# Kernel optimization log

Hardware: AMD Instinct MI355X
Metric: run time of the kernel (lower is better)

Reference implementation:

```python
import jax, jax.numpy as jnp
import numpy as np

D = 128          # cfg_node_encoding_dim
N_NODES = 300000
EPS = 1e-9


def setup_inputs() -> dict:
    key = jax.random.key(0)
    ks = jax.random.split(key, 10)
    inp = {
        "occ_ngram3": jax.random.normal(ks[0], (250000, 3, D), dtype=jnp.float32),
        "idx_ngram3": jax.random.randint(ks[1], (250000, 3), 0, N_NODES, dtype=jnp.int64),
        "occ_ngram5": jax.random.normal(ks[2], (200000, 5, D), dtype=jnp.float32),
        "idx_ngram5": jax.random.randint(ks[3], (200000, 5), 0, N_NODES, dtype=jnp.int64),
        "previous_cfg_nodes_encodings": jax.random.normal(ks[4], (N_NODES, D), dtype=jnp.float32),
        # learned params: attention key projection + GRU-like gate
        "attn_W": jax.random.normal(ks[5], (D, D), dtype=jnp.float32) / np.sqrt(D),
        "attn_b": jnp.zeros((D,), dtype=jnp.float32),
        "gate_W": jax.random.normal(ks[6], (2 * D, D), dtype=jnp.float32) / np.sqrt(2 * D),
        "gate_b": jnp.zeros((D,), dtype=jnp.float32),
        "nr_cfg_nodes": N_NODES,
    }
    return inp


def _scatter_attn_gate(occ3, occ5, prev, attn_W, attn_b, gate_W, gate_b, idx3, idx5, n_nodes):
    # flatten(0,1) + cat over sorted ngram lengths -> [E, D] values, [E] indices
    vals = jnp.concatenate([occ3.reshape(-1, D), occ5.reshape(-1, D)], axis=0)
    idx = jnp.concatenate([idx3.reshape(-1), idx5.reshape(-1)], axis=0)

    # scatter-attention keyed on previous node encodings
    keys = prev @ attn_W + attn_b                        # [N, D]
    scores = jnp.einsum('ed,ed->e', vals, keys[idx]) / jnp.sqrt(jnp.asarray(D, vals.dtype))
    seg_max = jax.ops.segment_max(scores, idx, num_segments=n_nodes)   # -inf for empty segs
    ex = jnp.exp(scores - seg_max[idx])
    denom = jax.ops.segment_sum(ex, idx, num_segments=n_nodes)
    probs = ex / (denom[idx] + EPS)                      # segment softmax [E]
    agg = jax.ops.segment_sum(probs[:, None] * vals, idx, num_segments=n_nodes)  # [N, D]

    # GRU-like gate: z = sigmoid(W [prev; update]); new = z*update + (1-z)*prev
    z = jax.nn.sigmoid(jnp.concatenate([prev, agg], axis=-1) @ gate_W + gate_b)
    return z * agg + (1.0 - z) * prev


def reference(occ_ngram3, idx_ngram3, occ_ngram5, idx_ngram5,
              previous_cfg_nodes_encodings, attn_W, attn_b, gate_W, gate_b,
              nr_cfg_nodes):
    return _scatter_attn_gate(occ_ngram3, occ_ngram5, previous_cfg_nodes_encodings,
                              attn_W, attn_b, gate_W, gate_b,
                              idx_ngram3, idx_ngram5, nr_cfg_nodes)
```

## Files before the change

### kernel.cpp

```cpp
#include <hip/hip_runtime.h>
#include <math.h>

#define D 128
#define EPSF 1e-9f

typedef __bf16 bf16x8 __attribute__((ext_vector_type(8)));
typedef float  f32x4  __attribute__((ext_vector_type(4)));
typedef float  f32x2  __attribute__((ext_vector_type(2)));

static __device__ __forceinline__ float bf2f(unsigned short h) {
    union { unsigned int u; float f; } c; c.u = ((unsigned int)h) << 16;
    return c.f;
}
static __device__ __forceinline__ unsigned short f2bf(float f) {
    union { float f; unsigned int u; } c; c.f = f;
    unsigned int u = c.u + 0x7fffu + ((c.u >> 16) & 1u);
    return (unsigned short)(u >> 16);
}

__global__ __launch_bounds__(256) void transpose_w_kernel(
    const float* __restrict__ attn_W, const float* __restrict__ gate_W,
    __bf16* __restrict__ wta, __bf16* __restrict__ wtg)
{
    int i = blockIdx.x * 256 + threadIdx.x;
    if (i < 128 * 128) {
        int k = i >> 7, n = i & 127;
        wta[n * 128 + k] = (__bf16)attn_W[i];
    }
    if (i < 256 * 128) {
        int k = i >> 7, n = i & 127;
        wtg[n * 256 + k] = (__bf16)gate_W[i];
    }
}

__global__ __launch_bounds__(256) void keys_mfma_kernel(
    const float* __restrict__ prev, const __bf16* __restrict__ wta,
    const float* __restrict__ attn_b, unsigned short* __restrict__ keysb, int N)
{
    const int lane = threadIdx.x & 63;
    const int wid  = threadIdx.x >> 6;
    const int m0 = (blockIdx.x * 4 + wid) * 16;
    if (m0 >= N) return;
    const int lm = lane & 15;
    const int lg = lane >> 4;

    int arow = m0 + lm; if (arow >= N) arow = m0;
    const float* ap = prev + (size_t)arow * D + lg * 8;

    f32x4 acc[8] = {};
    #pragma unroll
    for (int kk = 0; kk < 4; ++kk) {
        float4 a0 = *(const float4*)(ap + kk * 32);
        float4 a1 = *(const float4*)(ap + kk * 32 + 4);
        bf16x8 af;
        af[0] = (__bf16)a0.x; af[1] = (__bf16)a0.y; af[2] = (__bf16)a0.z; af[3] = (__bf16)a0.w;
        af[4] = (__bf16)a1.x; af[5] = (__bf16)a1.y; af[6] = (__bf16)a1.z; af[7] = (__bf16)a1.w;
        const int k0 = kk * 32;
        #pragma unroll
        for (int t = 0; t < 8; ++t) {
            bf16x8 bf_ = *(const bf16x8*)(wta + (size_t)(t * 16 + lm) * 128 + k0 + lg * 8);
            acc[t] = __builtin_amdgcn_mfma_f32_16x16x32_bf16(af, bf_, acc[t], 0, 0, 0);
        }
    }
    __bf16* kb = (__bf16*)keysb;
    #pragma unroll
    for (int t = 0; t < 8; ++t) {
        float bcol = attn_b[t * 16 + lm];
        #pragma unroll
        for (int r = 0; r < 4; ++r) {
            int row = m0 + lg * 4 + r;
            if (row < N)
                kb[(size_t)row * D + t * 16 + lm] = (__bf16)(acc[t][r] + bcol);
        }
    }
}

__global__ __launch_bounds__(256) void hist_kernel(
    const int* __restrict__ idx3, const int* __restrict__ idx5,
    int* __restrict__ cnt, int E3, int E)
{
    int e = blockIdx.x * 256 + threadIdx.x;
    if (e >= E) return;
    int n = (e < E3) ? idx3[e] : idx5[e - E3];
    atomicAdd(&cnt[n], 1);
}

__global__ __launch_bounds__(256) void scan1_kernel(
    const int* __restrict__ cnt, int* __restrict__ row_start,
    int* __restrict__ bsum, int N)
{
    __shared__ int tsum[256];
    const int t = threadIdx.x;
    const int base = blockIdx.x * 1024;
    const int i0 = base + t * 4;
    int v0 = 0, v1 = 0, v2 = 0, v3 = 0;
    if (i0 + 0 < N) v0 = cnt[i0 + 0];
    if (i0 + 1 < N) v1 = cnt[i0 + 1];
    if (i0 + 2 < N) v2 = cnt[i0 + 2];
    if (i0 + 3 < N) v3 = cnt[i0 + 3];
    int s = v0 + v1 + v2 + v3;
    tsum[t] = s;
    __syncthreads();
    int val = s;
    for (int off = 1; off < 256; off <<= 1) {
        int tmp = (t >= off) ? tsum[t - off] : 0;
        __syncthreads();
        val += tmp; tsum[t] = val;
        __syncthreads();
    }
    int excl = val - s;
    if (i0 + 0 < N) row_start[i0 + 0] = excl;            excl += v0;
    if (i0 + 1 < N) row_start[i0 + 1] = excl;            excl += v1;
    if (i0 + 2 < N) row_start[i0 + 2] = excl;            excl += v2;
    if (i0 + 3 < N) row_start[i0 + 3] = excl;
    if (t == 255) bsum[blockIdx.x] = val;
}

__global__ __launch_bounds__(1024) void scan2_kernel(int* __restrict__ bsum, int nb)
{
    __shared__ int sh[1024];
    const int t = threadIdx.x;
    int v = (t < nb) ? bsum[t] : 0;
    sh[t] = v;
    __syncthreads();
    int val = v;
    for (int off = 1; off < 1024; off <<= 1) {
        int tmp = (t >= off) ? sh[t - off] : 0;
        __syncthreads();
        val += tmp; sh[t] = val;
        __syncthreads();
    }
    if (t < nb) bsum[t] = val - v;
}

__global__ __launch_bounds__(256) void scan3_kernel(
    int* __restrict__ row_start, const int* __restrict__ bsum, int N, int E)
{
    int i = blockIdx.x * 256 + threadIdx.x;
    if (i < N)       row_start[i] += bsum[i >> 10];
    else if (i == N) row_start[N] = E;
}

__global__ __launch_bounds__(256) void scatter_kernel(
    const int* __restrict__ idx3, const int* __restrict__ idx5,
    const int* __restrict__ row_start, int* __restrict__ cursor,
    int* __restrict__ edge_ids, int E3, int E)
{
    int e = blockIdx.x * 256 + threadIdx.x;
    if (e >= E) return;
    int n = (e < E3) ? idx3[e] : idx5[e - E3];
    int p = row_start[n] + atomicAdd(&cursor[n], 1);
    edge_ids[p] = e;
}

__global__ __launch_bounds__(256) void agg_kernel(
    const float* __restrict__ occ3, const float* __restrict__ occ5,
    const unsigned short* __restrict__ keysb,
    const int* __restrict__ row_start, const int* __restrict__ edge_ids,
    unsigned int* __restrict__ aggb, int E3, int N)
{
    const int lane = threadIdx.x & 63;
    const int wid  = threadIdx.x >> 6;
    const int n = blockIdx.x * 4 + wid;
    if (n >= N) return;

    unsigned int kp = ((const unsigned int*)keysb)[(size_t)n * (D / 2) + lane];
    float kx = bf2f((unsigned short)(kp & 0xffffu));
    float ky = bf2f((unsigned short)(kp >> 16));

    const int rs = row_start[n];
    const int re = row_start[n + 1];
    const float scale = 0.0883883476483184f;

    float ax = 0.f, ay = 0.f, den = 0.f;

    for (int base = rs; base < re; base += 64) {
        const int nid = re - base;
        const int cnt = nid < 64 ? nid : 64;
        int myid = (lane < cnt) ? edge_ids[base + lane] : 0;

        for (int j0 = 0; j0 < cnt; j0 += 8) {
            f32x2 v[8];
            #pragma unroll
            for (int j = 0; j < 8; ++j) {
                int e = __shfl(myid, j0 + j);
                const f32x2* vp = (e < E3)
                    ? (const f32x2*)(occ3 + (size_t)e * D)
                    : (const f32x2*)(occ5 + (size_t)(e - E3) * D);
                v[j] = __builtin_nontemporal_load(&vp[lane]);
            }
            float s[8];
            #pragma unroll
            for (int j = 0; j < 8; ++j)
                s[j] = v[j][0] * kx + v[j][1] * ky;
            #pragma unroll
            for (int sh = 32; sh >= 1; sh >>= 1) {
                #pragma unroll
                for (int j = 0; j < 8; ++j)
                    s[j] += __shfl_xor(s[j], sh);
            }
            #pragma unroll
            for (int j = 0; j < 8; ++j) {
                float ex = (j0 + j < cnt) ? __expf(s[j] * scale) : 0.f;
                den += ex;
                ax = fmaf(ex, v[j][0], ax);
                ay = fmaf(ex, v[j][1], ay);
            }
        }
    }

    float inv = 1.0f / (den + EPSF);
    unsigned int pack = (unsigned int)f2bf(ax * inv)
                      | ((unsigned int)f2bf(ay * inv) << 16);
    aggb[(size_t)n * (D / 2) + lane] = pack;
}

__global__ __launch_bounds__(256) void gate_mfma_kernel(
    const float* __restrict__ prev, const __bf16* __restrict__ aggb,
    const __bf16* __restrict__ wtg, const float* __restrict__ gate_b,
    float* __restrict__ out, int N)
{
    const int lane = threadIdx.x & 63;
    const int wid  = threadIdx.x >> 6;
    const int m0 = (blockIdx.x * 4 + wid) * 16;
    if (m0 >= N) return;
    const int lm = lane & 15;
    const int lg = lane >> 4;

    int arow = m0 + lm; if (arow >= N) arow = m0;
    const float*  aprev = prev + (size_t)arow * D + lg * 8;
    const __bf16* aagg  = aggb + (size_t)arow * D + lg * 8;

    f32x4 acc[8] = {};
    #pragma unroll
    for (int kk = 0; kk < 4; ++kk) {
        float4 a0 = *(const float4*)(aprev + kk * 32);
        float4 a1 = *(const float4*)(aprev + kk * 32 + 4);
        bf16x8 af;
        af[0] = (__bf16)a0.x; af[1] = (__bf16)a0.y; af[2] = (__bf16)a0.z; af[3] = (__bf16)a0.w;
        af[4] = (__bf16)a1.x; af[5] = (__bf16)a1.y; af[6] = (__bf16)a1.z; af[7] = (__bf16)a1.w;
        const int k0 = kk * 32;
        #pragma unroll
        for (int t = 0; t < 8; ++t) {
            bf16x8 bf_ = *(const bf16x8*)(wtg + (size_t)(t * 16 + lm) * 256 + k0 + lg * 8);
            acc[t] = __builtin_amdgcn_mfma_f32_16x16x32_bf16(af, bf_, acc[t], 0, 0, 0);
        }
    }
    #pragma unroll
    for (int kk = 0; kk < 4; ++kk) {
        bf16x8 af = *(const bf16x8*)(aagg + kk * 32);
        const int k0 = 128 + kk * 32;
        #pragma unroll
        for (int t = 0; t < 8; ++t) {
            bf16x8 bf_ = *(const bf16x8*)(wtg + (size_t)(t * 16 + lm) * 256 + k0 + lg * 8);
            acc[t] = __builtin_amdgcn_mfma_f32_16x16x32_bf16(af, bf_, acc[t], 0, 0, 0);
        }
    }

    const unsigned short* aggu = (const unsigned short*)aggb;
    #pragma unroll
    for (int t = 0; t < 8; ++t) {
        float bcol = gate_b[t * 16 + lm];
        #pragma unroll
        for (int r = 0; r < 4; ++r) {
            int row = m0 + lg * 4 + r;
            if (row < N) {
                size_t off = (size_t)row * D + t * 16 + lm;
                float c = acc[t][r] + bcol;
                float z = 1.0f / (1.0f + __expf(-c));
                float a = bf2f(aggu[off]);
                float p = prev[off];
                out[off] = fmaf(z, a - p, p);
            }
        }
    }
}

extern "C" void kernel_launch(void* const* d_in, const int* in_sizes, int n_in,
                              void* d_out, int out_size, void* d_ws, size_t ws_size,
                              hipStream_t stream)
{
    const float* occ3   = (const float*)d_in[0];
    const int*   idx3   = (const int*)d_in[1];
    const float* occ5   = (const float*)d_in[2];
    const int*   idx5   = (const int*)d_in[3];
    const float* prev   = (const float*)d_in[4];
    const float* attn_W = (const float*)d_in[5];
    const float* attn_b = (const float*)d_in[6];
    const float* gate_W = (const float*)d_in[7];
    const float* gate_b = (const float*)d_in[8];

    const int N  = in_sizes[4] / D;
    const int E3 = in_sizes[1];
    const int E5 = in_sizes[3];
    const int E  = E3 + E5;

    unsigned short* keysb = (unsigned short*)d_ws;
    unsigned int*   aggb  = (unsigned int*)(keysb + (size_t)N * D);
    int* row_start = (int*)((unsigned short*)aggb + (size_t)N * D);
    int* cnt       = row_start + (N + 1);
    int* cursor    = cnt + N;
    int* bsum      = cursor + N;
    int* edge_ids  = bsum + 1025;
    __bf16* wta    = (__bf16*)(edge_ids + E);
    __bf16* wtg    = wta + 128 * 128;

    float* out = (float*)d_out;

    (void)hipMemsetAsync(cnt, 0, (size_t)2 * N * sizeof(int), stream);

    transpose_w_kernel<<<128, 256, 0, stream>>>(attn_W, gate_W, wta, wtg);

    const int nb = (N + 1023) / 1024;
    hist_kernel   <<<(E + 255) / 256, 256, 0, stream>>>(idx3, idx5, cnt, E3, E);
    scan1_kernel  <<<nb, 256, 0, stream>>>(cnt, row_start, bsum, N);
    scan2_kernel  <<<1, 1024, 0, stream>>>(bsum, nb);
    scan3_kernel  <<<(N + 256) / 256, 256, 0, stream>>>(row_start, bsum, N, E);
    scatter_kernel<<<(E + 255) / 256, 256, 0, stream>>>(idx3, idx5, row_start, cursor, edge_ids, E3, E);

    keys_mfma_kernel<<<(N + 63) / 64, 256, 0, stream>>>(prev, wta, attn_b, keysb, N);

    agg_kernel<<<(N + 3) / 4, 256, 0, stream>>>(occ3, occ5, keysb, row_start, edge_ids, aggb, E3, N);

    gate_mfma_kernel<<<(N + 63) / 64, 256, 0, stream>>>(prev, (const __bf16*)aggb, wtg, gate_b, out, N);
}
```

Baseline: 792.1 us.

## Fuse key projection, segment aggregation and gate into one per-tile kernel

Replaces the separate keys, aggregation and gate kernels with one fused kernel. Each wavefront owns 16 consecutive nodes: it computes their keys with MFMA into LDS, walks the CSR edges of all 16 nodes together, accumulates softmax-weighted values with LDS atomics, normalizes, and then runs the gate MFMA reading aggregates from LDS. This removes the global round trips for the bf16 keys and aggregates plus two launches. In exchange it adds LDS atomics, a binary search per edge chunk, and fewer wavefronts for the memory-bound edge gather (one wave per 16 nodes instead of one per node), which may reduce latency hiding.

```diff
diff --git a/kernel.cpp b/kernel.cpp
--- a/kernel.cpp
+++ b/kernel.cpp
@@ -3,6 +3,7 @@
 
 #define D 128
 #define EPSF 1e-9f
+#define KST 136
 
 typedef __bf16 bf16x8 __attribute__((ext_vector_type(8)));
 typedef float  f32x4  __attribute__((ext_vector_type(4)));
@@ -30,48 +31,6 @@
     if (i < 256 * 128) {
         int k = i >> 7, n = i & 127;
         wtg[n * 256 + k] = (__bf16)gate_W[i];
-    }
-}
-
-__global__ __launch_bounds__(256) void keys_mfma_kernel(
-    const float* __restrict__ prev, const __bf16* __restrict__ wta,
-    const float* __restrict__ attn_b, unsigned short* __restrict__ keysb, int N)
-{
-    const int lane = threadIdx.x & 63;
-    const int wid  = threadIdx.x >> 6;
-    const int m0 = (blockIdx.x * 4 + wid) * 16;
-    if (m0 >= N) return;
-    const int lm = lane & 15;
-    const int lg = lane >> 4;
-
-    int arow = m0 + lm; if (arow >= N) arow = m0;
-    const float* ap = prev + (size_t)arow * D + lg * 8;
-
-    f32x4 acc[8] = {};
-    #pragma unroll
-    for (int kk = 0; kk < 4; ++kk) {
-        float4 a0 = *(const float4*)(ap + kk * 32);
-        float4 a1 = *(const float4*)(ap + kk * 32 + 4);
-        bf16x8 af;
-        af[0] = (__bf16)a0.x; af[1] = (__bf16)a0.y; af[2] = (__bf16)a0.z; af[3] = (__bf16)a0.w;
-        af[4] = (__bf16)a1.x; af[5] = (__bf16)a1.y; af[6] = (__bf16)a1.z; af[7] = (__bf16)a1.w;
-        const int k0 = kk * 32;
-        #pragma unroll
-        for (int t = 0; t < 8; ++t) {
-            bf16x8 bf_ = *(const bf16x8*)(wta + (size_t)(t * 16 + lm) * 128 + k0 + lg * 8);
-            acc[t] = __builtin_amdgcn_mfma_f32_16x16x32_bf16(af, bf_, acc[t], 0, 0, 0);
-        }
-    }
-    __bf16* kb = (__bf16*)keysb;
-    #pragma unroll
-    for (int t = 0; t < 8; ++t) {
-        float bcol = attn_b[t * 16 + lm];
-        #pragma unroll
-        for (int r = 0; r < 4; ++r) {
-            int row = m0 + lg * 4 + r;
-            if (row < N)
-                kb[(size_t)row * D + t * 16 + lm] = (__bf16)(acc[t][r] + bcol);
-        }
     }
 }
 
@@ -153,73 +112,18 @@
     edge_ids[p] = e;
 }
 
-__global__ __launch_bounds__(256) void agg_kernel(
+__global__ __launch_bounds__(256) void fused_kernel(
+    const float* __restrict__ prev,
     const float* __restrict__ occ3, const float* __restrict__ occ5,
-    const unsigned short* __restrict__ keysb,
+    const __bf16* __restrict__ wta, const __bf16* __restrict__ wtg,
+    const float* __restrict__ attn_b, const float* __restrict__ gate_b,
     const int* __restrict__ row_start, const int* __restrict__ edge_ids,
-    unsigned int* __restrict__ aggb, int E3, int N)
-{
-    const int lane = threadIdx.x & 63;
-    const int wid  = threadIdx.x >> 6;
-    const int n = blockIdx.x * 4 + wid;
-    if (n >= N) return;
-
-    unsigned int kp = ((const unsigned int*)keysb)[(size_t)n * (D / 2) + lane];
-    float kx = bf2f((unsigned short)(kp & 0xffffu));
-    float ky = bf2f((unsigned short)(kp >> 16));
-
-    const int rs = row_start[n];
-    const int re = row_start[n + 1];
-    const float scale = 0.0883883476483184f;
-
-    float ax = 0.f, ay = 0.f, den = 0.f;
-
-    for (int base = rs; base < re; base += 64) {
-        const int nid = re - base;
-        const int cnt = nid < 64 ? nid : 64;
-        int myid = (lane < cnt) ? edge_ids[base + lane] : 0;
-
-        for (int j0 = 0; j0 < cnt; j0 += 8) {
-            f32x2 v[8];
-            #pragma unroll
-            for (int j = 0; j < 8; ++j) {
-                int e = __shfl(myid, j0 + j);
-                const f32x2* vp = (e < E3)
-                    ? (const f32x2*)(occ3 + (size_t)e * D)
-                    : (const f32x2*)(occ5 + (size_t)(e - E3) * D);
-                v[j] = __builtin_nontemporal_load(&vp[lane]);
-            }
-            float s[8];
-            #pragma unroll
-            for (int j = 0; j < 8; ++j)
-                s[j] = v[j][0] * kx + v[j][1] * ky;
-            #pragma unroll
-            for (int sh = 32; sh >= 1; sh >>= 1) {
-                #pragma unroll
-                for (int j = 0; j < 8; ++j)
-                    s[j] += __shfl_xor(s[j], sh);
-            }
-            #pragma unroll
-            for (int j = 0; j < 8; ++j) {
-                float ex = (j0 + j < cnt) ? __expf(s[j] * scale) : 0.f;
-                den += ex;
-                ax = fmaf(ex, v[j][0], ax);
-                ay = fmaf(ex, v[j][1], ay);
-            }
-        }
-    }
-
-    float inv = 1.0f / (den + EPSF);
-    unsigned int pack = (unsigned int)f2bf(ax * inv)
-                      | ((unsigned int)f2bf(ay * inv) << 16);
-    aggb[(size_t)n * (D / 2) + lane] = pack;
-}
-
-__global__ __launch_bounds__(256) void gate_mfma_kernel(
-    const float* __restrict__ prev, const __bf16* __restrict__ aggb,
-    const __bf16* __restrict__ wtg, const float* __restrict__ gate_b,
-    float* __restrict__ out, int N)
-{
+    float* __restrict__ out, int E3, int N)
+{
+    __shared__ __bf16 kag[4][16 * KST];
+    __shared__ float  agf[4][16 * D];
+    __shared__ float  dnf[4][16];
+
     const int lane = threadIdx.x & 63;
     const int wid  = threadIdx.x >> 6;
     const int m0 = (blockIdx.x * 4 + wid) * 16;
@@ -227,50 +131,140 @@
     const int lm = lane & 15;
     const int lg = lane >> 4;
 
+    __bf16* kl = kag[wid];
+    float*  af = agf[wid];
+    float*  dn = dnf[wid];
+
+    for (int i = lane; i < 16 * D; i += 64) af[i] = 0.f;
+    if (lane < 16) dn[lane] = 0.f;
+
     int arow = m0 + lm; if (arow >= N) arow = m0;
-    const float*  aprev = prev + (size_t)arow * D + lg * 8;
-    const __bf16* aagg  = aggb + (size_t)arow * D + lg * 8;
-
-    f32x4 acc[8] = {};
+    const float* ap = prev + (size_t)arow * D + lg * 8;
+    {
+        f32x4 acc[8] = {};
+        #pragma unroll
+        for (int kk = 0; kk < 4; ++kk) {
+            float4 a0 = *(const float4*)(ap + kk * 32);
+            float4 a1 = *(const float4*)(ap + kk * 32 + 4);
+            bf16x8 afr;
+            afr[0] = (__bf16)a0.x; afr[1] = (__bf16)a0.y; afr[2] = (__bf16)a0.z; afr[3] = (__bf16)a0.w;
+            afr[4] = (__bf16)a1.x; afr[5] = (__bf16)a1.y; afr[6] = (__bf16)a1.z; afr[7] = (__bf16)a1.w;
+            const int k0 = kk * 32;
+            #pragma unroll
+            for (int t = 0; t < 8; ++t) {
+                bf16x8 bfr = *(const bf16x8*)(wta + (size_t)(t * 16 + lm) * 128 + k0 + lg * 8);
+                acc[t] = __builtin_amdgcn_mfma_f32_16x16x32_bf16(afr, bfr, acc[t], 0, 0, 0);
+            }
+        }
+        #pragma unroll
+        for (int t = 0; t < 8; ++t) {
+            float b = attn_b[t * 16 + lm];
+            #pragma unroll
+            for (int r = 0; r < 4; ++r)
+                kl[(lg * 4 + r) * KST + t * 16 + lm] = (__bf16)(acc[t][r] + b);
+        }
+    }
+
+    const int rs0 = row_start[m0];
+    int hi = m0 + 16; if (hi > N) hi = N;
+    const int re0 = row_start[hi];
+    int bidx = m0 + (lane < 16 ? lane : 16); if (bidx > N) bidx = N;
+    const int rsv = row_start[bidx];
+    const float scale = 0.0883883476483184f;
+
+    for (int base = rs0; base < re0; base += 64) {
+        int cnt = re0 - base; if (cnt > 64) cnt = 64;
+        int p = base + lane;
+        int myid = (lane < cnt) ? edge_ids[p] : 0;
+        int lo = 0;
+        #pragma unroll
+        for (int st = 8; st >= 1; st >>= 1) {
+            int v = __shfl(rsv, lo + st);
+            if (v <= p) lo += st;
+        }
+
+        for (int q0 = 0; q0 < cnt; q0 += 8) {
+            f32x2 v[8]; int nl[8]; float s[8];
+            #pragma unroll
+            for (int j = 0; j < 8; ++j) {
+                int e = __shfl(myid, q0 + j);
+                nl[j] = __shfl(lo, q0 + j);
+                const f32x2* vp = (e < E3)
+                    ? (const f32x2*)(occ3 + (size_t)e * D)
+                    : (const f32x2*)(occ5 + (size_t)(e - E3) * D);
+                v[j] = __builtin_nontemporal_load(&vp[lane]);
+            }
+            #pragma unroll
+            for (int j = 0; j < 8; ++j) {
+                unsigned int kp = *(const unsigned int*)(kl + nl[j] * KST + 2 * lane);
+                s[j] = v[j][0] * bf2f((unsigned short)(kp & 0xffffu))
+                     + v[j][1] * bf2f((unsigned short)(kp >> 16));
+            }
+            #pragma unroll
+            for (int sh = 32; sh >= 1; sh >>= 1) {
+                #pragma unroll
+                for (int j = 0; j < 8; ++j)
+                    s[j] += __shfl_xor(s[j], sh);
+            }
+            #pragma unroll
+            for (int j = 0; j < 8; ++j) {
+                float ex = (q0 + j < cnt) ? __expf(s[j] * scale) : 0.f;
+                atomicAdd(&af[nl[j] * D + 2 * lane],     ex * v[j][0]);
+                atomicAdd(&af[nl[j] * D + 2 * lane + 1], ex * v[j][1]);
+                if (lane == 0) atomicAdd(&dn[nl[j]], ex);
+            }
+        }
+    }
+    __threadfence_block();
+
+    #pragma unroll
+    for (int i = 0; i < 16; ++i) {
+        float inv = 1.0f / (dn[i] + EPSF);
+        float x = af[i * D + 2 * lane] * inv;
+        float y = af[i * D + 2 * lane + 1] * inv;
+        unsigned int pk = (unsigned int)f2bf(x) | ((unsigned int)f2bf(y) << 16);
+        *(unsigned int*)(kl + i * KST + 2 * lane) = pk;
+    }
+
+    f32x4 gacc[8] = {};
     #pragma unroll
     for (int kk = 0; kk < 4; ++kk) {
-        float4 a0 = *(const float4*)(aprev + kk * 32);
-        float4 a1 = *(const float4*)(aprev + kk * 32 + 4);
-        bf16x8 af;
-        af[0] = (__bf16)a0.x; af[1] = (__bf16)a0.y; af[2] = (__bf16)a0.z; af[3] = (__bf16)a0.w;
-        af[4] = (__bf16)a1.x; af[5] = (__bf16)a1.y; af[6] = (__bf16)a1.z; af[7] = (__bf16)a1.w;
+        float4 a0 = *(const float4*)(ap + kk * 32);
+        float4 a1 = *(const float4*)(ap + kk * 32 + 4);
+        bf16x8 afr;
+        afr[0] = (__bf16)a0.x; afr[1] = (__bf16)a0.y; afr[2] = (__bf16)a0.z; afr[3] = (__bf16)a0.w;
+        afr[4] = (__bf16)a1.x; afr[5] = (__bf16)a1.y; afr[6] = (__bf16)a1.z; afr[7] = (__bf16)a1.w;
         const int k0 = kk * 32;
         #pragma unroll
         for (int t = 0; t < 8; ++t) {
-            bf16x8 bf_ = *(const bf16x8*)(wtg + (size_t)(t * 16 + lm) * 256 + k0 + lg * 8);
-            acc[t] = __builtin_amdgcn_mfma_f32_16x16x32_bf16(af, bf_, acc[t], 0, 0, 0);
+            bf16x8 bfr = *(const bf16x8*)(wtg + (size_t)(t * 16 + lm) * 256 + k0 + lg * 8);
+            gacc[t] = __builtin_amdgcn_mfma_f32_16x16x32_bf16(afr, bfr, gacc[t], 0, 0, 0);
         }
     }
     #pragma unroll
     for (int kk = 0; kk < 4; ++kk) {
-        bf16x8 af = *(const bf16x8*)(aagg + kk * 32);
+        bf16x8 afr = *(const bf16x8*)(kl + lm * KST + kk * 32 + lg * 8);
         const int k0 = 128 + kk * 32;
         #pragma unroll
         for (int t = 0; t < 8; ++t) {
-            bf16x8 bf_ = *(const bf16x8*)(wtg + (size_t)(t * 16 + lm) * 256 + k0 + lg * 8);
-            acc[t] = __builtin_amdgcn_mfma_f32_16x16x32_bf16(af, bf_, acc[t], 0, 0, 0);
-        }
-    }
-
-    const unsigned short* aggu = (const unsigned short*)aggb;
+            bf16x8 bfr = *(const bf16x8*)(wtg + (size_t)(t * 16 + lm) * 256 + k0 + lg * 8);
+            gacc[t] = __builtin_amdgcn_mfma_f32_16x16x32_bf16(afr, bfr, gacc[t], 0, 0, 0);
+        }
+    }
+
     #pragma unroll
     for (int t = 0; t < 8; ++t) {
-        float bcol = gate_b[t * 16 + lm];
+        float bc = gate_b[t * 16 + lm];
         #pragma unroll
         for (int r = 0; r < 4; ++r) {
             int row = m0 + lg * 4 + r;
             if (row < N) {
                 size_t off = (size_t)row * D + t * 16 + lm;
-                float c = acc[t][r] + bcol;
+                float c = gacc[t][r] + bc;
                 float z = 1.0f / (1.0f + __expf(-c));
-                float a = bf2f(aggu[off]);
-                float p = prev[off];
-                out[off] = fmaf(z, a - p, p);
+                float a = bf2f(*(const unsigned short*)(kl + (lg * 4 + r) * KST + t * 16 + lm));
+                float pv = prev[off];
+                out[off] = fmaf(z, a - pv, pv);
             }
         }
     }
@@ -295,9 +289,7 @@
     const int E5 = in_sizes[3];
     const int E  = E3 + E5;
 
-    unsigned short* keysb = (unsigned short*)d_ws;
-    unsigned int*   aggb  = (unsigned int*)(keysb + (size_t)N * D);
-    int* row_start = (int*)((unsigned short*)aggb + (size_t)N * D);
+    int* row_start = (int*)d_ws;
     int* cnt       = row_start + (N + 1);
     int* cursor    = cnt + N;
     int* bsum      = cursor + N;
@@ -318,9 +310,6 @@
     scan3_kernel  <<<(N + 256) / 256, 256, 0, stream>>>(row_start, bsum, N, E);
     scatter_kernel<<<(E + 255) / 256, 256, 0, stream>>>(idx3, idx5, row_start, cursor, edge_ids, E3, E);
 
-    keys_mfma_kernel<<<(N + 63) / 64, 256, 0, stream>>>(prev, wta, attn_b, keysb, N);
-
-    agg_kernel<<<(N + 3) / 4, 256, 0, stream>>>(occ3, occ5, keysb, row_start, edge_ids, aggb, E3, N);
-
-    gate_mfma_kernel<<<(N + 63) / 64, 256, 0, stream>>>(prev, (const __bf16*)aggb, wtg, gate_b, out, N);
-}
+    fused_kernel<<<(N + 63) / 64, 256, 0, stream>>>(
+        prev, occ3, occ5, wta, wtg, attn_b, gate_b, row_start, edge_ids, out, E3, N);
+}
```

Result: slower. 1.649 ms (+108.2%).
